# Optimization experiments

Hardware: AMD Instinct MI355X
Metric: run time of the kernel (lower is better)

Reference implementation:

```python
import jax, jax.numpy as jnp
import numpy as np

B, N, D, H_DIM = 8, 100, 768, 768
TH = 24            # 384 / patch16
IMG = 384


def setup_inputs() -> dict:
    key = jax.random.key(0)
    k0, k1, k2, k3 = jax.random.split(key, 4)
    patch_tokens = jax.random.normal(k0, (B, TH * TH + 1, D), jnp.float32)
    raw = jax.random.uniform(k1, (B, N, 4), jnp.float32)
    x1 = jnp.minimum(raw[..., 0], raw[..., 2])
    x2 = jnp.maximum(raw[..., 0], raw[..., 2])
    y1 = jnp.minimum(raw[..., 1], raw[..., 3])
    y2 = jnp.maximum(raw[..., 1], raw[..., 3])
    boxes = jnp.stack([x1, y1, x2, y2], axis=-1)
    W1 = jax.random.normal(k2, (2 * D, H_DIM), jnp.float32) * 0.02
    b1 = jnp.zeros((H_DIM,), jnp.float32)
    W2 = jax.random.normal(k3, (H_DIM, 1), jnp.float32) * 0.02
    b2 = jnp.zeros((1,), jnp.float32)
    return {"patch_tokens": patch_tokens, "boxes": boxes, "W1": W1, "b1": b1,
            "W2": W2, "b2": b2, "img_h": IMG, "img_w": IMG}


def reference(patch_tokens, boxes, W1, b1, W2, b2, img_h, img_w):
    Bt, T, Dm = patch_tokens.shape
    th = int(T ** 0.5)                       # token_hw (24 for T=577)
    seq = patch_tokens[:, 1:, :] if T == th * th + 1 else patch_tokens
    feat_map = seq.reshape(Bt, th, th, Dm)   # [B, th, th, D]

    # --- box -> patch-grid coordinates (replicates int() truncation chain) ---
    def to_patch(v, size):
        pix = jnp.floor(v * size)            # int(x * W), x >= 0
        return jnp.floor(pix / size * th).astype(jnp.int32)

    px1 = jnp.clip(to_patch(boxes[..., 0], img_w), 0, th - 1)  # [B, N]
    py1 = jnp.clip(to_patch(boxes[..., 1], img_h), 0, th - 1)
    px2 = jnp.clip(to_patch(boxes[..., 2], img_w), 1, th)
    py2 = jnp.clip(to_patch(boxes[..., 3], img_h), 1, th)
    # empty-region fallback: single cell at (py1, px1)
    px2 = jnp.where(px2 > px1, px2, px1 + 1)
    py2 = jnp.where(py2 > py1, py2, py1 + 1)

    # --- vectorized ROI mean pooling via rectangle masks ---
    ar = jnp.arange(th)
    mx = (ar[None, None, :] >= px1[..., None]) & (ar[None, None, :] < px2[..., None])  # [B,N,th]
    my = (ar[None, None, :] >= py1[..., None]) & (ar[None, None, :] < py2[..., None])  # [B,N,th]
    mask = (my[..., :, None] & mx[..., None, :]).astype(feat_map.dtype)               # [B,N,th,th]
    count = mask.sum(axis=(-1, -2))                                                   # [B,N]
    pooled = jnp.einsum('bnhw,bhwd->bnd', mask, feat_map) / count[..., None]          # [B,N,D]

    # --- pairwise concat-MLP: cat([fi, fj]) @ W1 == fi @ W1[:D] + fj @ W1[D:] ---
    ha = pooled @ W1[:Dm]                     # [B,N,H]
    hb = pooled @ W1[Dm:]                     # [B,N,H]
    hid = jax.nn.relu(ha[:, :, None, :] + hb[:, None, :, :] + b1)  # [B,N,N,H]
    logits = (hid @ W2)[..., 0] + b2[0]       # [B,N,N]
    return jax.nn.sigmoid(logits)
```

## Files before the change

### kernel.cpp

```cpp
#include <hip/hip_runtime.h>
#include <hip/hip_bf16.h>
#include <math.h>

#define PB   8
#define PN   100
#define PD   768
#define PT   577
#define PTH  24
#define BN_TOT (PB * PN)
#define MPAD   832

typedef __attribute__((ext_vector_type(8))) short bf16x8;
typedef __attribute__((ext_vector_type(4))) float f32x4;

__global__ __launch_bounds__(256) void sat_x_kernel(
    const float* __restrict__ patch,
    float* __restrict__ SAT)
{
    const int idx = blockIdx.x * 256 + threadIdx.x;
    const int d = idx % PD;
    const int y = (idx / PD) % PTH;
    const int b = idx / (PD * PTH);

    const float* src = patch + ((size_t)(b * PT + 1 + y * PTH)) * PD + d;
    float* dst = SAT + ((size_t)((b * 25) + (y + 1)) * 25) * PD + d;

    dst[0] = 0.0f;
    float acc = 0.0f;
#pragma unroll
    for (int X = 1; X <= PTH; ++X) {
        acc += src[(size_t)(X - 1) * PD];
        dst[(size_t)X * PD] = acc;
    }
}

__global__ __launch_bounds__(256) void sat_y_kernel(float* __restrict__ SAT)
{
    const int idx = blockIdx.x * 256 + threadIdx.x;
    const int d = idx % PD;
    const int X = (idx / PD) % 25;
    const int b = idx / (PD * 25);

    float* col = SAT + ((size_t)(b * 25) * 25 + X) * PD + d;
    col[0] = 0.0f;
    float acc = 0.0f;
#pragma unroll
    for (int Y = 1; Y <= PTH; ++Y) {
        float* p = col + (size_t)Y * 25 * PD;
        acc += *p;
        *p = acc;
    }
}

__global__ __launch_bounds__(256) void cvt_w1t_kernel(
    const float* __restrict__ W1, __hip_bfloat16* __restrict__ W1T)
{
    __shared__ float tile[32][33];
    const int half = blockIdx.z;
    const int k0 = blockIdx.y * 32;
    const int n0 = blockIdx.x * 32;
    const int c = threadIdx.x & 31;
    const int r4 = threadIdx.x >> 5;

#pragma unroll
    for (int l = 0; l < 4; ++l) {
        int r = r4 + 8 * l;
        tile[r][c] = W1[(size_t)(half * PD + k0 + r) * PD + n0 + c];
    }
    __syncthreads();
#pragma unroll
    for (int l = 0; l < 4; ++l) {
        int r = r4 + 8 * l;
        float v = tile[c][r];
        W1T[(size_t)(half * PD + n0 + r) * PD + k0 + c] = __float2bfloat16(v);
    }
}

__global__ __launch_bounds__(256) void pool_sat_kernel(
    const float* __restrict__ SAT,
    const float* __restrict__ boxes,
    const int*   __restrict__ img_h,
    const int*   __restrict__ img_w,
    __hip_bfloat16* __restrict__ pooledh)
{
    const int m = blockIdx.x;
    const int t = threadIdx.x;
    __hip_bfloat16* o = pooledh + (size_t)m * PD;

    if (m >= BN_TOT) {
        o[t] = __float2bfloat16(0.0f);
        o[t + 256] = __float2bfloat16(0.0f);
        o[t + 512] = __float2bfloat16(0.0f);
        return;
    }

    const int b = m / PN;
    const float x1 = boxes[m * 4 + 0];
    const float y1 = boxes[m * 4 + 1];
    const float x2 = boxes[m * 4 + 2];
    const float y2 = boxes[m * 4 + 3];
    const float W  = (float)img_w[0];
    const float H  = (float)img_h[0];

    auto to_patch = [](float v, float size) -> int {
        float pix = floorf(v * size);
        float tt  = pix / size * (float)PTH;
        return (int)floorf(tt);
    };
    int px1 = min(max(to_patch(x1, W), 0), PTH - 1);
    int py1 = min(max(to_patch(y1, H), 0), PTH - 1);
    int px2 = min(max(to_patch(x2, W), 1), PTH);
    int py2 = min(max(to_patch(y2, H), 1), PTH);
    if (px2 <= px1) px2 = px1 + 1;
    if (py2 <= py1) py2 = py1 + 1;
    const float inv = 1.0f / (float)((px2 - px1) * (py2 - py1));

    const float* Sb = SAT + (size_t)b * 25 * 25 * PD;
    const float* S22 = Sb + ((size_t)py2 * 25 + px2) * PD;
    const float* S12 = Sb + ((size_t)py1 * 25 + px2) * PD;
    const float* S21 = Sb + ((size_t)py2 * 25 + px1) * PD;
    const float* S11 = Sb + ((size_t)py1 * 25 + px1) * PD;

#pragma unroll
    for (int l = 0; l < 3; ++l) {
        int d = t + l * 256;
        float s = (S22[d] - S12[d]) - (S21[d] - S11[d]);
        o[d] = __float2bfloat16(s * inv);
    }
}

__global__ __launch_bounds__(128) void gemm_mfma_kernel(
    const __hip_bfloat16* __restrict__ A,
    const __hip_bfloat16* __restrict__ Bt,
    const float* __restrict__ b1,
    float* __restrict__ C)
{
    const int bn = blockIdx.x;
    const int bm = blockIdx.y;
    const int wave = threadIdx.x >> 6;
    const int lane = threadIdx.x & 63;
    const int lm = lane & 15;
    const int g  = lane >> 4;

    const int m0 = bm * 32;
    const int n0 = bn * 64 + wave * 32;

    const __hip_bfloat16* pa0 = A  + (size_t)(m0 + lm) * PD + g * 8;
    const __hip_bfloat16* pa1 = pa0 + (size_t)16 * PD;
    const __hip_bfloat16* pb0 = Bt + (size_t)(n0 + lm) * PD + g * 8;
    const __hip_bfloat16* pb1 = pb0 + (size_t)16 * PD;

    f32x4 acc00 = {}, acc01 = {}, acc10 = {}, acc11 = {};

#pragma unroll 4
    for (int k0 = 0; k0 < PD; k0 += 32) {
        bf16x8 a0 = *(const bf16x8*)(pa0 + k0);
        bf16x8 a1 = *(const bf16x8*)(pa1 + k0);
        bf16x8 b0 = *(const bf16x8*)(pb0 + k0);
        bf16x8 b1v = *(const bf16x8*)(pb1 + k0);
        acc00 = __builtin_amdgcn_mfma_f32_16x16x32_bf16(a0, b0,  acc00, 0, 0, 0);
        acc01 = __builtin_amdgcn_mfma_f32_16x16x32_bf16(a0, b1v, acc01, 0, 0, 0);
        acc10 = __builtin_amdgcn_mfma_f32_16x16x32_bf16(a1, b0,  acc10, 0, 0, 0);
        acc11 = __builtin_amdgcn_mfma_f32_16x16x32_bf16(a1, b1v, acc11, 0, 0, 0);
    }

    const int rbase = g * 4;
#pragma unroll
    for (int r = 0; r < 4; ++r) {
        int row0 = m0 + rbase + r;
        int row1 = row0 + 16;
        int col0 = n0 + lm;
        int col1 = col0 + 16;
        float bb0 = (col0 < PD) ? b1[col0] : 0.0f;
        float bb1 = (col1 < PD) ? b1[col1] : 0.0f;
        C[(size_t)row0 * 1536 + col0] = acc00[r] + bb0;
        C[(size_t)row0 * 1536 + col1] = acc01[r] + bb1;
        C[(size_t)row1 * 1536 + col0] = acc10[r] + bb0;
        C[(size_t)row1 * 1536 + col1] = acc11[r] + bb1;
    }
}

__global__ __launch_bounds__(256) void pair_kernel(
    const float* __restrict__ hab,
    const float* __restrict__ W2,
    const float* __restrict__ b2,
    float* __restrict__ out)
{
    const int bn = blockIdx.x;
    const int b  = bn / PN;
    const int t  = threadIdx.x;
    const int wave = t >> 6;
    const int lane = t & 63;

    const float4* ha = (const float4*)(hab + (size_t)bn * 1536);
    const float4 sa0 = ha[lane], sa1 = ha[lane + 64], sa2 = ha[lane + 128];
    const float4* w2v = (const float4*)W2;
    const float4 w0 = w2v[lane], w1 = w2v[lane + 64], w2 = w2v[lane + 128];
    const float bb2 = b2[0];

    const float4* hbbase = (const float4*)(hab + (size_t)(b * PN) * 1536) + 192;

    int j = wave;
    const float4* hb = hbbase + (size_t)j * 384;
    float4 h0 = hb[lane], h1 = hb[lane + 64], h2 = hb[lane + 128];

    for (int s = 0; s < 25; ++s) {
        const float4 c0 = h0, c1 = h1, c2 = h2;
        const int jn = j + 4;
        if (s < 24) {
            const float4* hbn = hbbase + (size_t)jn * 384;
            h0 = hbn[lane]; h1 = hbn[lane + 64]; h2 = hbn[lane + 128];
        }
        float acc = 0.0f;
        acc = fmaf(fmaxf(sa0.x + c0.x, 0.0f), w0.x, acc);
        acc = fmaf(fmaxf(sa0.y + c0.y, 0.0f), w0.y, acc);
        acc = fmaf(fmaxf(sa0.z + c0.z, 0.0f), w0.z, acc);
        acc = fmaf(fmaxf(sa0.w + c0.w, 0.0f), w0.w, acc);
        acc = fmaf(fmaxf(sa1.x + c1.x, 0.0f), w1.x, acc);
        acc = fmaf(fmaxf(sa1.y + c1.y, 0.0f), w1.y, acc);
        acc = fmaf(fmaxf(sa1.z + c1.z, 0.0f), w1.z, acc);
        acc = fmaf(fmaxf(sa1.w + c1.w, 0.0f), w1.w, acc);
        acc = fmaf(fmaxf(sa2.x + c2.x, 0.0f), w2.x, acc);
        acc = fmaf(fmaxf(sa2.y + c2.y, 0.0f), w2.y, acc);
        acc = fmaf(fmaxf(sa2.z + c2.z, 0.0f), w2.z, acc);
        acc = fmaf(fmaxf(sa2.w + c2.w, 0.0f), w2.w, acc);
#pragma unroll
        for (int mask = 32; mask > 0; mask >>= 1)
            acc += __shfl_xor(acc, mask, 64);
        if (lane == 0)
            out[(size_t)bn * PN + j] = 1.0f / (1.0f + expf(-(acc + bb2)));
        j = jn;
    }
}

extern "C" void kernel_launch(void* const* d_in, const int* in_sizes, int n_in,
                              void* d_out, int out_size, void* d_ws, size_t ws_size,
                              hipStream_t stream) {
    const float* patch = (const float*)d_in[0];
    const float* boxes = (const float*)d_in[1];
    const float* W1    = (const float*)d_in[2];
    const float* b1    = (const float*)d_in[3];
    const float* W2    = (const float*)d_in[4];
    const float* b2    = (const float*)d_in[5];
    const int*   img_h = (const int*)d_in[6];
    const int*   img_w = (const int*)d_in[7];
    float* out = (float*)d_out;

    char* wsb = (char*)d_ws;
    float*          SAT     = (float*)(wsb);
    __hip_bfloat16* pooledh = (__hip_bfloat16*)(wsb + 15360000);
    __hip_bfloat16* W1T     = (__hip_bfloat16*)(wsb + 15360000 + 1277952);
    float*          hab     = (float*)(wsb + 15360000 + 1277952 + 2359296);

    sat_x_kernel<<<576, 256, 0, stream>>>(patch, SAT);
    cvt_w1t_kernel<<<dim3(24, 24, 2), 256, 0, stream>>>(W1, W1T);
    sat_y_kernel<<<600, 256, 0, stream>>>(SAT);
    pool_sat_kernel<<<MPAD, 256, 0, stream>>>(SAT, boxes, img_h, img_w, pooledh);
    gemm_mfma_kernel<<<dim3(24, 26), 128, 0, stream>>>(pooledh, W1T, b1, hab);
    pair_kernel<<<BN_TOT, 256, 0, stream>>>(hab, W2, b2, out);
}
```

Before: 130.1 us.

## Fuse SAT-x with W1 transpose, vectorize SAT/pool, tile pair kernel over rows

Merges the SAT x-prefix pass and the W1 transpose/convert into one launch, cutting one kernel launch. The SAT passes and the pooling kernel now use float4 loads and stores, and pooling writes packed bf16 vectors. The pair kernel now handles 8 query rows per block, so each loaded hb vector is reused across 8 rows instead of one, which cuts global reads. The cost is more registers per thread and fewer blocks for the SAT passes.

```diff
diff --git a/kernel.cpp b/kernel.cpp
--- a/kernel.cpp
+++ b/kernel.cpp
@@ -13,70 +13,79 @@
 typedef __attribute__((ext_vector_type(8))) short bf16x8;
 typedef __attribute__((ext_vector_type(4))) float f32x4;
 
-__global__ __launch_bounds__(256) void sat_x_kernel(
+#define SATX_BLOCKS 144
+#define CVT_BLOCKS  1152
+
+__global__ __launch_bounds__(256) void prep_kernel(
     const float* __restrict__ patch,
-    float* __restrict__ SAT)
-{
-    const int idx = blockIdx.x * 256 + threadIdx.x;
-    const int d = idx % PD;
-    const int y = (idx / PD) % PTH;
-    const int b = idx / (PD * PTH);
-
-    const float* src = patch + ((size_t)(b * PT + 1 + y * PTH)) * PD + d;
-    float* dst = SAT + ((size_t)((b * 25) + (y + 1)) * 25) * PD + d;
-
-    dst[0] = 0.0f;
-    float acc = 0.0f;
-#pragma unroll
-    for (int X = 1; X <= PTH; ++X) {
-        acc += src[(size_t)(X - 1) * PD];
-        dst[(size_t)X * PD] = acc;
+    const float* __restrict__ W1,
+    float* __restrict__ SAT,
+    __hip_bfloat16* __restrict__ W1T)
+{
+    __shared__ float tile[32][33];
+    const int t = threadIdx.x;
+
+    if (blockIdx.x < SATX_BLOCKS) {
+        const int gid = blockIdx.x * 256 + t;
+        const int d4 = gid % 192;
+        const int y  = (gid / 192) % PTH;
+        const int b  = gid / (192 * PTH);
+
+        const float4* src = (const float4*)(patch + ((size_t)(b * PT + 1 + y * PTH)) * PD) + d4;
+        float4* dst = (float4*)(SAT + ((size_t)((b * 25) + (y + 1)) * 25) * PD) + d4;
+
+        dst[0] = make_float4(0.f, 0.f, 0.f, 0.f);
+        float4 acc = make_float4(0.f, 0.f, 0.f, 0.f);
+#pragma unroll
+        for (int X = 1; X <= PTH; ++X) {
+            float4 v = src[(size_t)(X - 1) * 192];
+            acc.x += v.x; acc.y += v.y; acc.z += v.z; acc.w += v.w;
+            dst[(size_t)X * 192] = acc;
+        }
+    } else {
+        const int bid = blockIdx.x - SATX_BLOCKS;
+        const int half = bid / 576;
+        const int rem  = bid % 576;
+        const int k0 = (rem / 24) * 32;
+        const int n0 = (rem % 24) * 32;
+        const int c  = t & 31;
+        const int r4 = t >> 5;
+
+#pragma unroll
+        for (int l = 0; l < 4; ++l) {
+            int r = r4 + 8 * l;
+            tile[r][c] = W1[(size_t)(half * PD + k0 + r) * PD + n0 + c];
+        }
+        __syncthreads();
+#pragma unroll
+        for (int l = 0; l < 4; ++l) {
+            int r = r4 + 8 * l;
+            W1T[(size_t)(half * PD + n0 + r) * PD + k0 + c] =
+                __float2bfloat16(tile[c][r]);
+        }
     }
 }
 
 __global__ __launch_bounds__(256) void sat_y_kernel(float* __restrict__ SAT)
 {
-    const int idx = blockIdx.x * 256 + threadIdx.x;
-    const int d = idx % PD;
-    const int X = (idx / PD) % 25;
-    const int b = idx / (PD * 25);
-
-    float* col = SAT + ((size_t)(b * 25) * 25 + X) * PD + d;
-    col[0] = 0.0f;
-    float acc = 0.0f;
+    const int gid = blockIdx.x * 256 + threadIdx.x;
+    const int d4 = gid % 192;
+    const int X  = (gid / 192) % 25;
+    const int b  = gid / (192 * 25);
+
+    float4* col = (float4*)(SAT + ((size_t)(b * 25) * 25 + X) * PD) + d4;
+    col[0] = make_float4(0.f, 0.f, 0.f, 0.f);
+    float4 acc = make_float4(0.f, 0.f, 0.f, 0.f);
 #pragma unroll
     for (int Y = 1; Y <= PTH; ++Y) {
-        float* p = col + (size_t)Y * 25 * PD;
-        acc += *p;
+        float4* p = col + (size_t)Y * 25 * 192;
+        float4 v = *p;
+        acc.x += v.x; acc.y += v.y; acc.z += v.z; acc.w += v.w;
         *p = acc;
     }
 }
 
-__global__ __launch_bounds__(256) void cvt_w1t_kernel(
-    const float* __restrict__ W1, __hip_bfloat16* __restrict__ W1T)
-{
-    __shared__ float tile[32][33];
-    const int half = blockIdx.z;
-    const int k0 = blockIdx.y * 32;
-    const int n0 = blockIdx.x * 32;
-    const int c = threadIdx.x & 31;
-    const int r4 = threadIdx.x >> 5;
-
-#pragma unroll
-    for (int l = 0; l < 4; ++l) {
-        int r = r4 + 8 * l;
-        tile[r][c] = W1[(size_t)(half * PD + k0 + r) * PD + n0 + c];
-    }
-    __syncthreads();
-#pragma unroll
-    for (int l = 0; l < 4; ++l) {
-        int r = r4 + 8 * l;
-        float v = tile[c][r];
-        W1T[(size_t)(half * PD + n0 + r) * PD + k0 + c] = __float2bfloat16(v);
-    }
-}
-
-__global__ __launch_bounds__(256) void pool_sat_kernel(
+__global__ __launch_bounds__(192) void pool_sat_kernel(
     const float* __restrict__ SAT,
     const float* __restrict__ boxes,
     const int*   __restrict__ img_h,
@@ -85,12 +94,11 @@
 {
     const int m = blockIdx.x;
     const int t = threadIdx.x;
-    __hip_bfloat16* o = pooledh + (size_t)m * PD;
+    short4* o = (short4*)(pooledh + (size_t)m * PD);
 
     if (m >= BN_TOT) {
-        o[t] = __float2bfloat16(0.0f);
-        o[t + 256] = __float2bfloat16(0.0f);
-        o[t + 512] = __float2bfloat16(0.0f);
+        short4 z; z.x = 0; z.y = 0; z.z = 0; z.w = 0;
+        o[t] = z;
         return;
     }
 
@@ -116,17 +124,21 @@
     const float inv = 1.0f / (float)((px2 - px1) * (py2 - py1));
 
     const float* Sb = SAT + (size_t)b * 25 * 25 * PD;
-    const float* S22 = Sb + ((size_t)py2 * 25 + px2) * PD;
-    const float* S12 = Sb + ((size_t)py1 * 25 + px2) * PD;
-    const float* S21 = Sb + ((size_t)py2 * 25 + px1) * PD;
-    const float* S11 = Sb + ((size_t)py1 * 25 + px1) * PD;
-
-#pragma unroll
-    for (int l = 0; l < 3; ++l) {
-        int d = t + l * 256;
-        float s = (S22[d] - S12[d]) - (S21[d] - S11[d]);
-        o[d] = __float2bfloat16(s * inv);
-    }
+    const float4 s22 = ((const float4*)(Sb + ((size_t)py2 * 25 + px2) * PD))[t];
+    const float4 s12 = ((const float4*)(Sb + ((size_t)py1 * 25 + px2) * PD))[t];
+    const float4 s21 = ((const float4*)(Sb + ((size_t)py2 * 25 + px1) * PD))[t];
+    const float4 s11 = ((const float4*)(Sb + ((size_t)py1 * 25 + px1) * PD))[t];
+
+    auto cvt = [](float f) -> short {
+        __hip_bfloat16 h = __float2bfloat16(f);
+        return *(short*)&h;
+    };
+    short4 r;
+    r.x = cvt(((s22.x - s12.x) - (s21.x - s11.x)) * inv);
+    r.y = cvt(((s22.y - s12.y) - (s21.y - s11.y)) * inv);
+    r.z = cvt(((s22.z - s12.z) - (s21.z - s11.z)) * inv);
+    r.w = cvt(((s22.w - s12.w) - (s21.w - s11.w)) * inv);
+    o[t] = r;
 }
 
 __global__ __launch_bounds__(128) void gemm_mfma_kernel(
@@ -180,56 +192,74 @@
     }
 }
 
+__device__ __forceinline__ float rdot(const float4 A, const float4 C,
+                                      const float4 W, float s) {
+    s = fmaf(fmaxf(A.x + C.x, 0.f), W.x, s);
+    s = fmaf(fmaxf(A.y + C.y, 0.f), W.y, s);
+    s = fmaf(fmaxf(A.z + C.z, 0.f), W.z, s);
+    s = fmaf(fmaxf(A.w + C.w, 0.f), W.w, s);
+    return s;
+}
+
 __global__ __launch_bounds__(256) void pair_kernel(
     const float* __restrict__ hab,
     const float* __restrict__ W2,
     const float* __restrict__ b2,
     float* __restrict__ out)
 {
-    const int bn = blockIdx.x;
-    const int b  = bn / PN;
-    const int t  = threadIdx.x;
+    const int jt = blockIdx.x;
+    const int i0 = blockIdx.y * 8;
+    const int b  = blockIdx.z;
+    const int nrows = min(8, PN - i0);
+    const int t = threadIdx.x;
     const int wave = t >> 6;
     const int lane = t & 63;
 
-    const float4* ha = (const float4*)(hab + (size_t)bn * 1536);
-    const float4 sa0 = ha[lane], sa1 = ha[lane + 64], sa2 = ha[lane + 128];
     const float4* w2v = (const float4*)W2;
-    const float4 w0 = w2v[lane], w1 = w2v[lane + 64], w2 = w2v[lane + 128];
+    const float4 w0 = w2v[lane], w1 = w2v[lane + 64], w2r = w2v[lane + 128];
     const float bb2 = b2[0];
 
+    float4 a[8][3];
+#pragma unroll
+    for (int i = 0; i < 8; ++i) {
+        int row = b * PN + (i < nrows ? i0 + i : i0);
+        const float4* ha = (const float4*)(hab + (size_t)row * 1536);
+        a[i][0] = ha[lane]; a[i][1] = ha[lane + 64]; a[i][2] = ha[lane + 128];
+    }
+
     const float4* hbbase = (const float4*)(hab + (size_t)(b * PN) * 1536) + 192;
-
-    int j = wave;
-    const float4* hb = hbbase + (size_t)j * 384;
-    float4 h0 = hb[lane], h1 = hb[lane + 64], h2 = hb[lane + 128];
-
-    for (int s = 0; s < 25; ++s) {
+    const int jend = jt * 50 + 50;
+    int j = jt * 50 + wave;
+
+    float4 h0, h1, h2;
+    {
+        const float4* hb = hbbase + (size_t)j * 384;
+        h0 = hb[lane]; h1 = hb[lane + 64]; h2 = hb[lane + 128];
+    }
+
+    for (; j < jend; j += 4) {
         const float4 c0 = h0, c1 = h1, c2 = h2;
         const int jn = j + 4;
-        if (s < 24) {
-            const float4* hbn = hbbase + (size_t)jn * 384;
-            h0 = hbn[lane]; h1 = hbn[lane + 64]; h2 = hbn[lane + 128];
-        }
-        float acc = 0.0f;
-        acc = fmaf(fmaxf(sa0.x + c0.x, 0.0f), w0.x, acc);
-        acc = fmaf(fmaxf(sa0.y + c0.y, 0.0f), w0.y, acc);
-        acc = fmaf(fmaxf(sa0.z + c0.z, 0.0f), w0.z, acc);
-        acc = fmaf(fmaxf(sa0.w + c0.w, 0.0f), w0.w, acc);
-        acc = fmaf(fmaxf(sa1.x + c1.x, 0.0f), w1.x, acc);
-        acc = fmaf(fmaxf(sa1.y + c1.y, 0.0f), w1.y, acc);
-        acc = fmaf(fmaxf(sa1.z + c1.z, 0.0f), w1.z, acc);
-        acc = fmaf(fmaxf(sa1.w + c1.w, 0.0f), w1.w, acc);
-        acc = fmaf(fmaxf(sa2.x + c2.x, 0.0f), w2.x, acc);
-        acc = fmaf(fmaxf(sa2.y + c2.y, 0.0f), w2.y, acc);
-        acc = fmaf(fmaxf(sa2.z + c2.z, 0.0f), w2.z, acc);
-        acc = fmaf(fmaxf(sa2.w + c2.w, 0.0f), w2.w, acc);
-#pragma unroll
-        for (int mask = 32; mask > 0; mask >>= 1)
-            acc += __shfl_xor(acc, mask, 64);
-        if (lane == 0)
-            out[(size_t)bn * PN + j] = 1.0f / (1.0f + expf(-(acc + bb2)));
-        j = jn;
+        if (jn < jend) {
+            const float4* hb = hbbase + (size_t)jn * 384;
+            h0 = hb[lane]; h1 = hb[lane + 64]; h2 = hb[lane + 128];
+        }
+        float acc[8];
+#pragma unroll
+        for (int i = 0; i < 8; ++i)
+            acc[i] = rdot(a[i][2], c2, w2r, rdot(a[i][1], c1, w1, rdot(a[i][0], c0, w0, 0.f)));
+#pragma unroll
+        for (int i = 0; i < 8; ++i)
+#pragma unroll
+            for (int m = 32; m; m >>= 1)
+                acc[i] += __shfl_xor(acc[i], m, 64);
+        if (lane == 0) {
+#pragma unroll
+            for (int i = 0; i < 8; ++i)
+                if (i < nrows)
+                    out[(size_t)(b * PN + i0 + i) * PN + j] =
+                        1.0f / (1.0f + expf(-(acc[i] + bb2)));
+        }
     }
 }
 
@@ -252,10 +282,9 @@
     __hip_bfloat16* W1T     = (__hip_bfloat16*)(wsb + 15360000 + 1277952);
     float*          hab     = (float*)(wsb + 15360000 + 1277952 + 2359296);
 
-    sat_x_kernel<<<576, 256, 0, stream>>>(patch, SAT);
-    cvt_w1t_kernel<<<dim3(24, 24, 2), 256, 0, stream>>>(W1, W1T);
-    sat_y_kernel<<<600, 256, 0, stream>>>(SAT);
-    pool_sat_kernel<<<MPAD, 256, 0, stream>>>(SAT, boxes, img_h, img_w, pooledh);
+    prep_kernel<<<SATX_BLOCKS + CVT_BLOCKS, 256, 0, stream>>>(patch, W1, SAT, W1T);
+    sat_y_kernel<<<150, 256, 0, stream>>>(SAT);
+    pool_sat_kernel<<<MPAD, 192, 0, stream>>>(SAT, boxes, img_h, img_w, pooledh);
     gemm_mfma_kernel<<<dim3(24, 26), 128, 0, stream>>>(pooledh, W1T, b1, hab);
-    pair_kernel<<<BN_TOT, 256, 0, stream>>>(hab, W2, b2, out);
-}
+    pair_kernel<<<dim3(2, 13, 8), 256, 0, stream>>>(hab, W2, b2, out);
+}
```

New measurement: 137.5 us. 1.06x slower.
